# Kernel tuning notes

Hardware: AMD Instinct MI355X
Metric: run time of the kernel (lower is better)

Reference implementation:

```python
import jax, jax.numpy as jnp
import numpy as np

N_NODES = 50000
N_EDGES = 800000
IN_FEATS = 256
HIDDEN = 256
NUM_CLASSES = 64


def setup_inputs() -> dict:
    key = jax.random.key(0)
    k1, k2, k3, k4 = jax.random.split(key, 4)
    features = jax.random.normal(k1, (N_NODES, IN_FEATS), dtype=jnp.float32)
    edge_index = jax.random.randint(k2, (2, N_EDGES), 0, N_NODES, dtype=jnp.int32)
    W1 = jax.random.normal(k3, (IN_FEATS, HIDDEN), dtype=jnp.float32) * (1.0 / np.sqrt(IN_FEATS))
    b1 = jnp.zeros((HIDDEN,), dtype=jnp.float32)
    W2 = jax.random.normal(k4, (HIDDEN, NUM_CLASSES), dtype=jnp.float32) * (1.0 / np.sqrt(HIDDEN))
    b2 = jnp.zeros((NUM_CLASSES,), dtype=jnp.float32)
    return {"features": features, "edge_index": edge_index, "W1": W1, "b1": b1, "W2": W2, "b2": b2}


def reference(features, edge_index, W1, b1, W2, b2):
    # Two-layer GCN: h = A_hat @ relu(A_hat @ X W1 + b1) W2 + b2
    # A_hat uses symmetric degree normalization 1/sqrt(d_src * d_dst)
    N = features.shape[0]
    src, dst = edge_index[0], edge_index[1]
    ones = jnp.ones((src.shape[0],), dtype=features.dtype)
    deg_out = jax.ops.segment_sum(ones, src, num_segments=N)  # out-degree per node
    deg_in = jax.ops.segment_sum(ones, dst, num_segments=N)   # in-degree per node
    inv_sqrt_out = jax.lax.rsqrt(jnp.maximum(deg_out, 1.0))
    inv_sqrt_in = jax.lax.rsqrt(jnp.maximum(deg_in, 1.0))
    edge_norm = (inv_sqrt_out[src] * inv_sqrt_in[dst])[:, None]  # [E,1]

    def gcn_layer(x, W, b):
        h = x @ W                      # transform first (reduces message width)
        msg = h[src] * edge_norm       # [E, out]
        agg = jax.ops.segment_sum(msg, dst, num_segments=N)
        return agg + b

    h = jax.nn.relu(gcn_layer(features, W1, b1))
    return gcn_layer(h, W2, b2)
```

## Files before the change

kernel.cpp:

```cpp
#include <hip/hip_runtime.h>

#define NN 50000
#define MPAD 50048
#define NE 800000
#define SCAN_BLOCKS 49

typedef short short8 __attribute__((ext_vector_type(8)));
typedef float f32x4 __attribute__((ext_vector_type(4)));

__device__ __forceinline__ unsigned short f2bf(float x) {
    unsigned u = __builtin_bit_cast(unsigned, x);
    u += 0x7FFFu + ((u >> 16) & 1u);
    return (unsigned short)(u >> 16);
}
__device__ __forceinline__ float bf2f(unsigned short h) {
    unsigned u = ((unsigned)h) << 16;
    return __builtin_bit_cast(float, u);
}
__device__ __forceinline__ void gld16(const void* g, void* l) {
    __builtin_amdgcn_global_load_lds(
        (const __attribute__((address_space(1))) unsigned int*)g,
        (__attribute__((address_space(3))) unsigned int*)l, 16, 0, 0);
}
__device__ __forceinline__ void nt_store8(void* p, ushort4 v) {
    __builtin_nontemporal_store(__builtin_bit_cast(unsigned long long, v),
                                (unsigned long long*)p);
}


__global__ __launch_bounds__(256) void count_kernel(const int* __restrict__ src,
    const int* __restrict__ dst, int* __restrict__ cnt_out, int* __restrict__ cnt_in, int E)
{
    int e = blockIdx.x * 256 + threadIdx.x;
    if (e < E) {
        atomicAdd(&cnt_out[src[e]], 1);
        atomicAdd(&cnt_in[dst[e]], 1);
    }
}

__global__ __launch_bounds__(256) void scan_kernel(const int* __restrict__ cnt_in,
    const int* __restrict__ cnt_out, int* __restrict__ bsum, int* __restrict__ rs,
    float* __restrict__ inv_out, float* __restrict__ inv_in)
{
    __shared__ int sm[4];
    __shared__ int sprefix;
    const int b = blockIdx.x, tid = threadIdx.x;
    const int lane = tid & 63, wv = tid >> 6;
    int base = b * 1024 + tid * 4;
    int v[4]; int s = 0;
    #pragma unroll
    for (int i = 0; i < 4; ++i) {
        int idx = base + i;
        v[i] = (idx < NN) ? cnt_in[idx] : 0;
        s += v[i];
    }
    int inc = s;
    #pragma unroll
    for (int off = 1; off < 64; off <<= 1) {
        int u = __shfl_up(inc, off, 64);
        if (lane >= off) inc += u;
    }
    if (lane == 63) sm[wv] = inc;
    __syncthreads();
    if (tid == 0) {
        int btot = sm[0] + sm[1] + sm[2] + sm[3];
        atomicExch(&bsum[b], btot + 1);
    }
    if (tid < 64) {
        int pv = 0;
        if (lane < b) {
            int x;
            do { x = atomicAdd(&bsum[lane], 0); } while (x == 0);
            pv = x - 1;
        }
        #pragma unroll
        for (int off = 1; off < 64; off <<= 1) pv += __shfl_xor(pv, off, 64);
        if (lane == 0) sprefix = pv;
    }
    __syncthreads();
    int wo = 0;
    for (int i = 0; i < wv; ++i) wo += sm[i];
    int run = sprefix + wo + (inc - s);
    #pragma unroll
    for (int i = 0; i < 4; ++i) {
        int idx = base + i;
        if (idx < NN) {
            rs[idx] = run; run += v[i];
            inv_in[idx]  = rsqrtf(fmaxf((float)v[i], 1.0f));
            inv_out[idx] = rsqrtf(fmaxf((float)cnt_out[idx], 1.0f));
        }
    }
}

__global__ __launch_bounds__(256) void fill_kernel(const int* __restrict__ src,
    const int* __restrict__ dst, int* __restrict__ rs, int* __restrict__ csr_src, int E)
{
    int e = blockIdx.x * 256 + threadIdx.x;
    if (e < E) {
        int slot = atomicAdd(&rs[dst[e]], 1);
        csr_src[slot] = src[e];
    }
}

__global__ __launch_bounds__(256) void splitW_kernel(const float* __restrict__ W1,
    const float* __restrict__ W2, unsigned short* __restrict__ W1T,
    unsigned short* __restrict__ W2T)
{
    int i = blockIdx.x * 256 + threadIdx.x;
    const float* W; unsigned short* BT; int N; int ii;
    if (i < 256 * 32) { W = W1; BT = W1T; N = 256; ii = i; }
    else if (i < 256 * 32 + 64 * 32) { W = W2; BT = W2T; N = 64; ii = i - 256 * 32; }
    else return;
    int col = ii >> 5, kc = ii & 31;
    short8 hv, lv;
    #pragma unroll
    for (int j = 0; j < 8; ++j) {
        float x = W[(size_t)(kc * 8 + j) * N + col];
        unsigned short h = f2bf(x);
        hv[j] = (short)h;
        lv[j] = (short)f2bf(x - bf2f(h));
    }
    size_t base = (size_t)col * 512;
    size_t o = (kc >> 3) * 64 + (((kc & 7) ^ (col & 7)) * 8);
    *(short8*)&BT[base + o] = hv;
    *(short8*)&BT[base + 256 + o] = lv;
}

__global__ __launch_bounds__(256) void gemm1_fuse_kernel(const float* __restrict__ X,
    const unsigned short* __restrict__ BT, const float* __restrict__ inv_out,
    unsigned short* __restrict__ C, int M)
{
    constexpr int BN = 128, WN = 64, NF = 4;
    __shared__ unsigned short Ash[128 * 64];
    __shared__ unsigned short Asl[128 * 64];
    __shared__ unsigned short Bsh[BN * 64];
    __shared__ unsigned short Bsl[BN * 64];
    const int tid = threadIdx.x;
    const int w = tid >> 6, lane = tid & 63;
    const int wm = w >> 1, wn = w & 1;
    const int r = lane & 15, kg = lane >> 4;
    const int rowbase = blockIdx.x * 128;
    const int colbase = blockIdx.y * BN;

    f32x4 acc[4][NF] = {};

    for (int kb = 0; kb < 4; ++kb) {
        #pragma unroll
        for (int i = 0; i < 4; ++i) {
            int ct = (w * 4 + i) * 64 + lane;
            int row = ct >> 3, c = ct & 7;
            int grow = rowbase + row; if (grow >= NN) grow = NN - 1;
            const float* sp = X + (size_t)grow * 256 + kb * 64 + c * 8;
            float4 x0 = *(const float4*)sp;
            float4 x1 = *(const float4*)(sp + 4);
            float xs[8] = {x0.x, x0.y, x0.z, x0.w, x1.x, x1.y, x1.z, x1.w};
            short8 hv, lv;
            #pragma unroll
            for (int t = 0; t < 8; ++t) {
                unsigned short h = f2bf(xs[t]);
                hv[t] = (short)h;
                lv[t] = (short)f2bf(xs[t] - bf2f(h));
            }
            int dsto = row * 64 + ((c ^ (row & 7)) * 8);
            *(short8*)&Ash[dsto] = hv;
            *(short8*)&Asl[dsto] = lv;
        }
        #pragma unroll
        for (int i = 0; i < 4; ++i) {
            int ct = (w * 4 + i) * 64 + lane;
            int col = ct >> 3, c = ct & 7;
            size_t goff = (size_t)(colbase + col) * 512 + kb * 64 + c * 8;
            gld16(BT + goff, (unsigned short*)Bsh + (size_t)ct * 8);
            gld16(BT + goff + 256, (unsigned short*)Bsl + (size_t)ct * 8);
        }
        __syncthreads();
        #pragma unroll
        for (int ks = 0; ks < 2; ++ks) {
            short8 ahf[4], alf[4];
            #pragma unroll
            for (int mf = 0; mf < 4; ++mf) {
                int row = wm * 64 + mf * 16 + r;
                int lo = row * 64 + (((ks * 4 + kg) ^ (row & 7)) * 8);
                ahf[mf] = *(const short8*)&Ash[lo];
                alf[mf] = *(const short8*)&Asl[lo];
            }
            #pragma unroll
            for (int nf = 0; nf < NF; ++nf) {
                int col = wn * WN + nf * 16 + r;
                int lo = col * 64 + (((ks * 4 + kg) ^ (col & 7)) * 8);
                short8 bh = *(const short8*)&Bsh[lo];
                short8 bl = *(const short8*)&Bsl[lo];
                #pragma unroll
                for (int mf = 0; mf < 4; ++mf) {
                    acc[mf][nf] = __builtin_amdgcn_mfma_f32_16x16x32_bf16(ahf[mf], bh, acc[mf][nf], 0, 0, 0);
                    acc[mf][nf] = __builtin_amdgcn_mfma_f32_16x16x32_bf16(alf[mf], bh, acc[mf][nf], 0, 0, 0);
                    acc[mf][nf] = __builtin_amdgcn_mfma_f32_16x16x32_bf16(ahf[mf], bl, acc[mf][nf], 0, 0, 0);
                }
            }
        }
        __syncthreads();
    }

    #pragma unroll
    for (int mf = 0; mf < 4; ++mf) {
        #pragma unroll
        for (int reg = 0; reg < 4; ++reg) {
            int orow = rowbase + wm * 64 + mf * 16 + kg * 4 + reg;
            if (orow >= M) continue;
            float sc = inv_out[orow];
            #pragma unroll
            for (int nf = 0; nf < NF; ++nf) {
                int ocol = colbase + wn * WN + nf * 16 + r;
                C[(size_t)orow * 256 + ocol] = f2bf(acc[mf][nf][reg] * sc);
            }
        }
    }
}

__global__ __launch_bounds__(256) void gemm2_kernel(
    const unsigned short* __restrict__ Ah, const unsigned short* __restrict__ Al,
    const unsigned short* __restrict__ BT, const float* __restrict__ inv_out,
    unsigned short* __restrict__ C, int M)
{
    constexpr int BN = 64, WN = 32, NF = 2, BI = 2;
    __shared__ unsigned short Ash[128 * 64];
    __shared__ unsigned short Asl[128 * 64];
    __shared__ unsigned short Bsh[BN * 64];
    __shared__ unsigned short Bsl[BN * 64];
    const int tid = threadIdx.x;
    const int w = tid >> 6, lane = tid & 63;
    const int wm = w >> 1, wn = w & 1;
    const int r = lane & 15, kg = lane >> 4;
    const int rowbase = blockIdx.x * 128;

    f32x4 acc[4][NF] = {};

    for (int kb = 0; kb < 4; ++kb) {
        #pragma unroll
        for (int i = 0; i < 4; ++i) {
            int ct = (w * 4 + i) * 64 + lane;
            int row = ct >> 3, c = ct & 7;
            size_t goff = (size_t)(rowbase + row) * 256 + kb * 64 + c * 8;
            gld16(Ah + goff, (unsigned short*)Ash + (size_t)ct * 8);
            gld16(Al + goff, (unsigned short*)Asl + (size_t)ct * 8);
        }
        #pragma unroll
        for (int i = 0; i < BI; ++i) {
            int ct = (w * BI + i) * 64 + lane;
            int col = ct >> 3, c = ct & 7;
            size_t goff = (size_t)col * 512 + kb * 64 + c * 8;
            gld16(BT + goff, (unsigned short*)Bsh + (size_t)ct * 8);
            gld16(BT + goff + 256, (unsigned short*)Bsl + (size_t)ct * 8);
        }
        __syncthreads();
        #pragma unroll
        for (int ks = 0; ks < 2; ++ks) {
            short8 ahf[4], alf[4];
            #pragma unroll
            for (int mf = 0; mf < 4; ++mf) {
                int row = wm * 64 + mf * 16 + r;
                int lo = row * 64 + (((ks * 4 + kg) ^ (row & 7)) * 8);
                ahf[mf] = *(const short8*)&Ash[lo];
                alf[mf] = *(const short8*)&Asl[lo];
            }
            #pragma unroll
            for (int nf = 0; nf < NF; ++nf) {
                int col = wn * WN + nf * 16 + r;
                int lo = col * 64 + (((ks * 4 + kg) ^ (col & 7)) * 8);
                short8 bh = *(const short8*)&Bsh[lo];
                short8 bl = *(const short8*)&Bsl[lo];
                #pragma unroll
                for (int mf = 0; mf < 4; ++mf) {
                    acc[mf][nf] = __builtin_amdgcn_mfma_f32_16x16x32_bf16(ahf[mf], bh, acc[mf][nf], 0, 0, 0);
                    acc[mf][nf] = __builtin_amdgcn_mfma_f32_16x16x32_bf16(alf[mf], bh, acc[mf][nf], 0, 0, 0);
                    acc[mf][nf] = __builtin_amdgcn_mfma_f32_16x16x32_bf16(ahf[mf], bl, acc[mf][nf], 0, 0, 0);
                }
            }
        }
        __syncthreads();
    }

    #pragma unroll
    for (int mf = 0; mf < 4; ++mf) {
        #pragma unroll
        for (int reg = 0; reg < 4; ++reg) {
            int orow = rowbase + wm * 64 + mf * 16 + kg * 4 + reg;
            if (orow >= M) continue;
            float sc = inv_out[orow];
            #pragma unroll
            for (int nf = 0; nf < NF; ++nf) {
                int ocol = wn * WN + nf * 16 + r;
                C[(size_t)orow * 64 + ocol] = f2bf(acc[mf][nf][reg] * sc);
            }
        }
    }
}

__global__ __launch_bounds__(256) void gather256_kernel(const unsigned short* __restrict__ t1,
    const int* __restrict__ csr_src, const int* __restrict__ rs,
    const float* __restrict__ inv_in, const float* __restrict__ b1,
    unsigned short* __restrict__ Ah2, unsigned short* __restrict__ Al2)
{
    int n = (int)((blockIdx.x * 256 + threadIdx.x) >> 6);
    int lane = threadIdx.x & 63;
    if (n >= NN) return;
    int begin = (n == 0) ? 0 : rs[n - 1];
    int end = rs[n];
    float a0 = 0.f, a1 = 0.f, a2 = 0.f, a3 = 0.f;
    int j = begin;
    for (; j + 8 <= end; j += 8) {
        int s0 = csr_src[j],     s1 = csr_src[j + 1], s2 = csr_src[j + 2], s3 = csr_src[j + 3];
        int s4 = csr_src[j + 4], s5 = csr_src[j + 5], s6 = csr_src[j + 6], s7 = csr_src[j + 7];
        ushort4 v0 = *(const ushort4*)&t1[(size_t)s0 * 256 + lane * 4];
        ushort4 v1 = *(const ushort4*)&t1[(size_t)s1 * 256 + lane * 4];
        ushort4 v2 = *(const ushort4*)&t1[(size_t)s2 * 256 + lane * 4];
        ushort4 v3 = *(const ushort4*)&t1[(size_t)s3 * 256 + lane * 4];
        ushort4 v4 = *(const ushort4*)&t1[(size_t)s4 * 256 + lane * 4];
        ushort4 v5 = *(const ushort4*)&t1[(size_t)s5 * 256 + lane * 4];
        ushort4 v6 = *(const ushort4*)&t1[(size_t)s6 * 256 + lane * 4];
        ushort4 v7 = *(const ushort4*)&t1[(size_t)s7 * 256 + lane * 4];
        a0 += bf2f(v0.x); a1 += bf2f(v0.y); a2 += bf2f(v0.z); a3 += bf2f(v0.w);
        a0 += bf2f(v1.x); a1 += bf2f(v1.y); a2 += bf2f(v1.z); a3 += bf2f(v1.w);
        a0 += bf2f(v2.x); a1 += bf2f(v2.y); a2 += bf2f(v2.z); a3 += bf2f(v2.w);
        a0 += bf2f(v3.x); a1 += bf2f(v3.y); a2 += bf2f(v3.z); a3 += bf2f(v3.w);
        a0 += bf2f(v4.x); a1 += bf2f(v4.y); a2 += bf2f(v4.z); a3 += bf2f(v4.w);
        a0 += bf2f(v5.x); a1 += bf2f(v5.y); a2 += bf2f(v5.z); a3 += bf2f(v5.w);
        a0 += bf2f(v6.x); a1 += bf2f(v6.y); a2 += bf2f(v6.z); a3 += bf2f(v6.w);
        a0 += bf2f(v7.x); a1 += bf2f(v7.y); a2 += bf2f(v7.z); a3 += bf2f(v7.w);
    }
    for (; j < end; ++j) {
        int s = csr_src[j];
        ushort4 v = *(const ushort4*)&t1[(size_t)s * 256 + lane * 4];
        a0 += bf2f(v.x); a1 += bf2f(v.y); a2 += bf2f(v.z); a3 += bf2f(v.w);
    }
    float win = inv_in[n];
    int f0 = lane * 4;
    float4 bb = *(const float4*)&b1[f0];
    float x0 = fmaxf(fmaf(a0, win, bb.x), 0.f);
    float x1 = fmaxf(fmaf(a1, win, bb.y), 0.f);
    float x2 = fmaxf(fmaf(a2, win, bb.z), 0.f);
    float x3 = fmaxf(fmaf(a3, win, bb.w), 0.f);
    unsigned short h0 = f2bf(x0), h1 = f2bf(x1), h2 = f2bf(x2), h3 = f2bf(x3);
    ushort4 hv = {h0, h1, h2, h3};
    ushort4 lv = {f2bf(x0 - bf2f(h0)), f2bf(x1 - bf2f(h1)),
                  f2bf(x2 - bf2f(h2)), f2bf(x3 - bf2f(h3))};
    int kb = f0 >> 6, c = (f0 >> 3) & 7, e = f0 & 7;
    size_t off = (size_t)n * 256 + kb * 64 + ((c ^ (n & 7)) * 8) + e;
    nt_store8(&Ah2[off], hv);
    nt_store8(&Al2[off], lv);
}

__global__ __launch_bounds__(256) void gather64_kernel(const unsigned short* __restrict__ t2,
    const int* __restrict__ csr_src, const int* __restrict__ rs,
    const float* __restrict__ inv_in, const float* __restrict__ b2,
    float* __restrict__ out)
{
    int n = (int)((blockIdx.x * 256 + threadIdx.x) >> 6);
    int lane = threadIdx.x & 63;
    if (n >= NN) return;
    int begin = (n == 0) ? 0 : rs[n - 1];
    int end = rs[n];
    float acc = 0.f;
    int j = begin;
    for (; j + 8 <= end; j += 8) {
        int s0 = csr_src[j],     s1 = csr_src[j + 1], s2 = csr_src[j + 2], s3 = csr_src[j + 3];
        int s4 = csr_src[j + 4], s5 = csr_src[j + 5], s6 = csr_src[j + 6], s7 = csr_src[j + 7];
        float v0 = bf2f(t2[(size_t)s0 * 64 + lane]);
        float v1 = bf2f(t2[(size_t)s1 * 64 + lane]);
        float v2 = bf2f(t2[(size_t)s2 * 64 + lane]);
        float v3 = bf2f(t2[(size_t)s3 * 64 + lane]);
        float v4 = bf2f(t2[(size_t)s4 * 64 + lane]);
        float v5 = bf2f(t2[(size_t)s5 * 64 + lane]);
        float v6 = bf2f(t2[(size_t)s6 * 64 + lane]);
        float v7 = bf2f(t2[(size_t)s7 * 64 + lane]);
        acc += v0; acc += v1; acc += v2; acc += v3;
        acc += v4; acc += v5; acc += v6; acc += v7;
    }
    for (; j < end; ++j) {
        int s = csr_src[j];
        acc += bf2f(t2[(size_t)s * 64 + lane]);
    }
    float o = fmaf(acc, inv_in[n], b2[lane]);
    __builtin_nontemporal_store(o, &out[(size_t)n * 64 + lane]);
}

extern "C" void kernel_launch(void* const* d_in, const int* in_sizes, int n_in,
                              void* d_out, int out_size, void* d_ws, size_t ws_size,
                              hipStream_t stream)
{
    const float* features = (const float*)d_in[0];
    const int*   edge_index = (const int*)d_in[1];
    const float* W1 = (const float*)d_in[2];
    const float* b1 = (const float*)d_in[3];
    const float* W2 = (const float*)d_in[4];
    const float* b2 = (const float*)d_in[5];
    float* out = (float*)d_out;
    const int* src = edge_index;
    const int* dst = edge_index + NE;

    char* p = (char*)d_ws;
    int* cnt_out = (int*)p;            p += (size_t)NN * 4;
    int* cnt_in  = (int*)p;            p += (size_t)NN * 4;
    int* bsum    = (int*)p;            p += 64 * 4;
    float* inv_out = (float*)p;        p += (size_t)NN * 4;
    float* inv_in  = (float*)p;        p += (size_t)NN * 4;
    int* rs      = (int*)p;            p += (size_t)NN * 4;
    int* csr_src = (int*)p;            p += (size_t)NE * 4;
    unsigned short* W1T = (unsigned short*)p;  p += (size_t)256 * 512 * 2;
    unsigned short* W2T = (unsigned short*)p;  p += (size_t)64 * 512 * 2;
    unsigned short* t1  = (unsigned short*)p;  p += (size_t)NN * 256 * 2;
    unsigned short* Ah2 = (unsigned short*)p;  p += (size_t)MPAD * 256 * 2;
    unsigned short* Al2 = (unsigned short*)p;  p += (size_t)MPAD * 256 * 2;
    unsigned short* t2  = (unsigned short*)p;  p += (size_t)NN * 64 * 2;

    hipMemsetAsync(cnt_out, 0, (2 * (size_t)NN + 64) * sizeof(int), stream);

    count_kernel<<<(NE + 255) / 256, 256, 0, stream>>>(src, dst, cnt_out, cnt_in, NE);
    scan_kernel<<<SCAN_BLOCKS, 256, 0, stream>>>(cnt_in, cnt_out, bsum, rs, inv_out, inv_in);
    fill_kernel<<<(NE + 255) / 256, 256, 0, stream>>>(src, dst, rs, csr_src, NE);

    splitW_kernel<<<(320 * 32 + 255) / 256, 256, 0, stream>>>(W1, W2, W1T, W2T);

    gemm1_fuse_kernel<<<dim3(MPAD / 128, 2), 256, 0, stream>>>(
        features, W1T, inv_out, t1, NN);

    gather256_kernel<<<(NN * 64 + 255) / 256, 256, 0, stream>>>(
        t1, csr_src, rs, inv_in, b1, Ah2, Al2);

    gemm2_kernel<<<MPAD / 128, 256, 0, stream>>>(
        Ah2, Al2, W2T, inv_out, t2, NN);

    gather64_kernel<<<(NN * 64 + 255) / 256, 256, 0, stream>>>(
        t2, csr_src, rs, inv_in, b2, out);
}
```

Baseline: 301.4 us.

## Privatize degree counters and CSR fill cursors per XCC, fold weight split into count

Degree counting and CSR slot assignment now use per-XCC private copies of the counter arrays, selected through the hardware XCC ID register. The atomics become workgroup-scope so they resolve in the local L2 rather than contending across dies. The scan merges the eight partial counts and writes per-XCC starting offsets so each XCC fills its own disjoint slot range. The weight-splitting kernel is folded into the count kernel to save a launch, and the row-start array gains a trailing entry so the gathers read begin and end directly. The cost is more memset traffic and eight reads per node in the scan. Correctness relies on workgroup-scope atomics being coherent among all blocks that run on the same XCC.

```diff
diff --git a/kernel.cpp b/kernel.cpp
--- a/kernel.cpp
+++ b/kernel.cpp
@@ -26,20 +26,47 @@
     __builtin_nontemporal_store(__builtin_bit_cast(unsigned long long, v),
                                 (unsigned long long*)p);
 }
-
+__device__ __forceinline__ unsigned xcc_id() {
+    unsigned x;
+    asm("s_getreg_b32 %0, hwreg(HW_REG_XCC_ID)" : "=s"(x));
+    return x & 7;
+}
 
 __global__ __launch_bounds__(256) void count_kernel(const int* __restrict__ src,
-    const int* __restrict__ dst, int* __restrict__ cnt_out, int* __restrict__ cnt_in, int E)
-{
+    const int* __restrict__ dst, int* __restrict__ cntp,
+    const float* __restrict__ W1, const float* __restrict__ W2,
+    unsigned short* __restrict__ W1T, unsigned short* __restrict__ W2T, int E)
+{
+    int* mycnt = cntp + (size_t)xcc_id() * (2 * NN);
     int e = blockIdx.x * 256 + threadIdx.x;
     if (e < E) {
-        atomicAdd(&cnt_out[src[e]], 1);
-        atomicAdd(&cnt_in[dst[e]], 1);
-    }
-}
-
-__global__ __launch_bounds__(256) void scan_kernel(const int* __restrict__ cnt_in,
-    const int* __restrict__ cnt_out, int* __restrict__ bsum, int* __restrict__ rs,
+        int s = src[e], d = dst[e];
+        __hip_atomic_fetch_add(&mycnt[s], 1, __ATOMIC_RELAXED, __HIP_MEMORY_SCOPE_WORKGROUP);
+        __hip_atomic_fetch_add(&mycnt[NN + d], 1, __ATOMIC_RELAXED, __HIP_MEMORY_SCOPE_WORKGROUP);
+    }
+    int i = blockIdx.x * 256 + threadIdx.x;
+    if (i < 320 * 32) {
+        const float* W; unsigned short* BT; int N; int ii;
+        if (i < 256 * 32) { W = W1; BT = W1T; N = 256; ii = i; }
+        else { W = W2; BT = W2T; N = 64; ii = i - 256 * 32; }
+        int col = ii >> 5, kc = ii & 31;
+        short8 hv, lv;
+        #pragma unroll
+        for (int j = 0; j < 8; ++j) {
+            float x = W[(size_t)(kc * 8 + j) * N + col];
+            unsigned short h = f2bf(x);
+            hv[j] = (short)h;
+            lv[j] = (short)f2bf(x - bf2f(h));
+        }
+        size_t base = (size_t)col * 512;
+        size_t o = (kc >> 3) * 64 + (((kc & 7) ^ (col & 7)) * 8);
+        *(short8*)&BT[base + o] = hv;
+        *(short8*)&BT[base + 256 + o] = lv;
+    }
+}
+
+__global__ __launch_bounds__(256) void scan_kernel(const int* __restrict__ cntp,
+    int* __restrict__ bsum, int* __restrict__ rs, int* __restrict__ rsp,
     float* __restrict__ inv_out, float* __restrict__ inv_in)
 {
     __shared__ int sm[4];
@@ -51,8 +78,13 @@
     #pragma unroll
     for (int i = 0; i < 4; ++i) {
         int idx = base + i;
-        v[i] = (idx < NN) ? cnt_in[idx] : 0;
-        s += v[i];
+        int t = 0;
+        if (idx < NN) {
+            #pragma unroll
+            for (int x = 0; x < 8; ++x)
+                t += cntp[(size_t)x * (2 * NN) + NN + idx];
+        }
+        v[i] = t; s += t;
     }
     int inc = s;
     #pragma unroll
@@ -85,45 +117,34 @@
     for (int i = 0; i < 4; ++i) {
         int idx = base + i;
         if (idx < NN) {
-            rs[idx] = run; run += v[i];
-            inv_in[idx]  = rsqrtf(fmaxf((float)v[i], 1.0f));
-            inv_out[idx] = rsqrtf(fmaxf((float)cnt_out[idx], 1.0f));
-        }
-    }
+            rs[idx] = run;
+            int rx = run;
+            #pragma unroll
+            for (int x = 0; x < 8; ++x) {
+                rsp[(size_t)x * NN + idx] = rx;
+                rx += cntp[(size_t)x * (2 * NN) + NN + idx];
+            }
+            run += v[i];
+            inv_in[idx] = rsqrtf(fmaxf((float)v[i], 1.0f));
+            int dout = 0;
+            #pragma unroll
+            for (int x = 0; x < 8; ++x) dout += cntp[(size_t)x * (2 * NN) + idx];
+            inv_out[idx] = rsqrtf(fmaxf((float)dout, 1.0f));
+        }
+    }
+    if (b == 0 && tid == 0) rs[NN] = NE;
 }
 
 __global__ __launch_bounds__(256) void fill_kernel(const int* __restrict__ src,
-    const int* __restrict__ dst, int* __restrict__ rs, int* __restrict__ csr_src, int E)
-{
+    const int* __restrict__ dst, int* __restrict__ rsp, int* __restrict__ csr_src, int E)
+{
+    int* myrs = rsp + (size_t)xcc_id() * NN;
     int e = blockIdx.x * 256 + threadIdx.x;
     if (e < E) {
-        int slot = atomicAdd(&rs[dst[e]], 1);
+        int slot = __hip_atomic_fetch_add(&myrs[dst[e]], 1, __ATOMIC_RELAXED,
+                                          __HIP_MEMORY_SCOPE_WORKGROUP);
         csr_src[slot] = src[e];
     }
-}
-
-__global__ __launch_bounds__(256) void splitW_kernel(const float* __restrict__ W1,
-    const float* __restrict__ W2, unsigned short* __restrict__ W1T,
-    unsigned short* __restrict__ W2T)
-{
-    int i = blockIdx.x * 256 + threadIdx.x;
-    const float* W; unsigned short* BT; int N; int ii;
-    if (i < 256 * 32) { W = W1; BT = W1T; N = 256; ii = i; }
-    else if (i < 256 * 32 + 64 * 32) { W = W2; BT = W2T; N = 64; ii = i - 256 * 32; }
-    else return;
-    int col = ii >> 5, kc = ii & 31;
-    short8 hv, lv;
-    #pragma unroll
-    for (int j = 0; j < 8; ++j) {
-        float x = W[(size_t)(kc * 8 + j) * N + col];
-        unsigned short h = f2bf(x);
-        hv[j] = (short)h;
-        lv[j] = (short)f2bf(x - bf2f(h));
-    }
-    size_t base = (size_t)col * 512;
-    size_t o = (kc >> 3) * 64 + (((kc & 7) ^ (col & 7)) * 8);
-    *(short8*)&BT[base + o] = hv;
-    *(short8*)&BT[base + 256 + o] = lv;
 }
 
 __global__ __launch_bounds__(256) void gemm1_fuse_kernel(const float* __restrict__ X,
@@ -304,8 +325,8 @@
     int n = (int)((blockIdx.x * 256 + threadIdx.x) >> 6);
     int lane = threadIdx.x & 63;
     if (n >= NN) return;
-    int begin = (n == 0) ? 0 : rs[n - 1];
-    int end = rs[n];
+    int begin = rs[n];
+    int end = rs[n + 1];
     float a0 = 0.f, a1 = 0.f, a2 = 0.f, a3 = 0.f;
     int j = begin;
     for (; j + 8 <= end; j += 8) {
@@ -358,8 +379,8 @@
     int n = (int)((blockIdx.x * 256 + threadIdx.x) >> 6);
     int lane = threadIdx.x & 63;
     if (n >= NN) return;
-    int begin = (n == 0) ? 0 : rs[n - 1];
-    int end = rs[n];
+    int begin = rs[n];
+    int end = rs[n + 1];
     float acc = 0.f;
     int j = begin;
     for (; j + 8 <= end; j += 8) {
@@ -399,12 +420,12 @@
     const int* dst = edge_index + NE;
 
     char* p = (char*)d_ws;
-    int* cnt_out = (int*)p;            p += (size_t)NN * 4;
-    int* cnt_in  = (int*)p;            p += (size_t)NN * 4;
-    int* bsum    = (int*)p;            p += 64 * 4;
+    int* cntp = (int*)p;               p += (size_t)8 * 2 * NN * 4;
+    int* bsum = (int*)p;               p += 64 * 4;
+    int* rs   = (int*)p;               p += (size_t)(NN + 1) * 4;
+    int* rsp  = (int*)p;               p += (size_t)8 * NN * 4;
     float* inv_out = (float*)p;        p += (size_t)NN * 4;
     float* inv_in  = (float*)p;        p += (size_t)NN * 4;
-    int* rs      = (int*)p;            p += (size_t)NN * 4;
     int* csr_src = (int*)p;            p += (size_t)NE * 4;
     unsigned short* W1T = (unsigned short*)p;  p += (size_t)256 * 512 * 2;
     unsigned short* W2T = (unsigned short*)p;  p += (size_t)64 * 512 * 2;
@@ -413,13 +434,12 @@
     unsigned short* Al2 = (unsigned short*)p;  p += (size_t)MPAD * 256 * 2;
     unsigned short* t2  = (unsigned short*)p;  p += (size_t)NN * 64 * 2;
 
-    hipMemsetAsync(cnt_out, 0, (2 * (size_t)NN + 64) * sizeof(int), stream);
-
-    count_kernel<<<(NE + 255) / 256, 256, 0, stream>>>(src, dst, cnt_out, cnt_in, NE);
-    scan_kernel<<<SCAN_BLOCKS, 256, 0, stream>>>(cnt_in, cnt_out, bsum, rs, inv_out, inv_in);
-    fill_kernel<<<(NE + 255) / 256, 256, 0, stream>>>(src, dst, rs, csr_src, NE);
-
-    splitW_kernel<<<(320 * 32 + 255) / 256, 256, 0, stream>>>(W1, W2, W1T, W2T);
+    hipMemsetAsync(cntp, 0, ((size_t)8 * 2 * NN + 64) * sizeof(int), stream);
+
+    count_kernel<<<(NE + 255) / 256, 256, 0, stream>>>(
+        src, dst, cntp, W1, W2, W1T, W2T, NE);
+    scan_kernel<<<SCAN_BLOCKS, 256, 0, stream>>>(cntp, bsum, rs, rsp, inv_out, inv_in);
+    fill_kernel<<<(NE + 255) / 256, 256, 0, stream>>>(src, dst, rsp, csr_src, NE);
 
     gemm1_fuse_kernel<<<dim3(MPAD / 128, 2), 256, 0, stream>>>(
         features, W1T, inv_out, t1, NN);
```

Result: no change. 297.9 us (median of 2 runs) (-1.2%).
